# Kernel optimization log

Measured on AMD Instinct MI355X. Metric: run time of the kernel, lower is better.

The kernel has to match this reference:

```python
import jax, jax.numpy as jnp
import numpy as np

N_NODES = 100000
N_EDGES = 1600000
MSG = 128
EPS = 1e-12  # F.normalize default eps


def setup_inputs() -> dict:
    key = jax.random.key(0)
    ks = jax.random.split(key, 12)
    s = 1.0 / np.sqrt(MSG)
    inp = {
        "x": jax.random.normal(ks[0], (N_NODES, 3), dtype=jnp.float32),
        "m_ij": jax.random.normal(ks[1], (N_EDGES, MSG), dtype=jnp.float32),
        "edges": jax.random.randint(ks[2], (2, N_EDGES), 0, N_NODES, dtype=jnp.int64),
        # weigths MLP: Linear(MSG,MSG) -> SiLU -> Linear(MSG,1)
        "Ww1": jax.random.uniform(ks[3], (MSG, MSG), jnp.float32, -s, s),
        "bw1": jax.random.uniform(ks[4], (MSG,), jnp.float32, -s, s),
        "Ww2": jax.random.uniform(ks[5], (MSG, 1), jnp.float32, -s, s),
        "bw2": jax.random.uniform(ks[6], (1,), jnp.float32, -s, s),
        # attention MLP: Linear(MSG,MSG) -> SiLU -> Linear(MSG,1)
        "Wa1": jax.random.uniform(ks[7], (MSG, MSG), jnp.float32, -s, s),
        "ba1": jax.random.uniform(ks[8], (MSG,), jnp.float32, -s, s),
        "Wa2": jax.random.uniform(ks[9], (MSG, 1), jnp.float32, -s, s),
        "ba2": jax.random.uniform(ks[10], (1,), jnp.float32, -s, s),
    }
    return inp


def reference(x, m_ij, edges, Ww1, bw1, Ww2, bw2, Wa1, ba1, Wa2, ba2):
    n_nodes = x.shape[0]
    src = edges[0]  # receiver index (scatter target)
    dst = edges[1]  # neighbor index

    # w_ij = MLP(m_ij) -> [E, 1]
    w_ij = jax.nn.silu(m_ij @ Ww1 + bw1) @ Ww2 + bw2

    # attention: a_ij = exp(MLP(m_ij)); normalized per receiver node (softmax-like)
    a_ij = jnp.exp(jax.nn.silu(m_ij @ Wa1 + ba1) @ Wa2 + ba2)  # [E, 1]
    a_i = jax.ops.segment_sum(a_ij, src, num_segments=n_nodes)  # [N, 1]
    w_ij = w_ij * (a_ij / a_i[src])

    # normalized position differences, weighted
    d = x[dst] - x[src]  # [E, 3]
    norm = jnp.maximum(jnp.linalg.norm(d, axis=1, keepdims=True), EPS)
    x_ij = (d / norm) * w_ij

    x_diff = jax.ops.segment_sum(x_ij, src, num_segments=n_nodes)  # [N, 3]
    return x + x_diff
```

## Files before the change

### kernel.cpp

```cpp
#include <hip/hip_runtime.h>
#include <cmath>

#define MSG 128
#define TILE_M 128

typedef __attribute__((ext_vector_type(8))) __bf16 bf16x8;
typedef __attribute__((ext_vector_type(4))) float f32x4;

__device__ __forceinline__ unsigned short f2bf(float f) {
  union { float f; unsigned u; } v; v.f = f;
  unsigned r = v.u + 0x7FFFu + ((v.u >> 16) & 1u);
  return (unsigned short)(r >> 16);
}

__global__ void prep_weights_kernel(const float* __restrict__ Ww1,
                                    const float* __restrict__ Wa1,
                                    unsigned short* __restrict__ WtW,
                                    unsigned short* __restrict__ WtA) {
  int idx = blockIdx.x * blockDim.x + threadIdx.x;
  if (idx < MSG * MSG) {
    int k = idx >> 7;
    int n = idx & 127;
    WtW[n * MSG + k] = f2bf(Ww1[idx]);
    WtA[n * MSG + k] = f2bf(Wa1[idx]);
  }
}

__global__ __launch_bounds__(256, 5)
void edge_mlp_fused_kernel(const float* __restrict__ m_ij,
                           const unsigned short* __restrict__ WtW,
                           const unsigned short* __restrict__ WtA,
                           const float* __restrict__ bw1, const float* __restrict__ Ww2,
                           const float* __restrict__ bw2,
                           const float* __restrict__ ba1, const float* __restrict__ Wa2,
                           const float* __restrict__ ba2,
                           const int* __restrict__ src,
                           const int* __restrict__ dst,
                           const float* __restrict__ x,
                           float* __restrict__ num4, int E) {
  const int tid = threadIdx.x;
  const int wv = tid >> 6;
  const int lane = tid & 63;
  const int quad = lane >> 4;
  const int l16 = lane & 15;
  const int ebase = blockIdx.x * TILE_M + wv * 32;

  const int eown = ebase + lane;
  const bool owner = (lane < 32) && (eown < E);
  int s = 0, d = 0;
  if (owner) { s = src[eown]; d = dst[eown]; }

  bf16x8 mfrag[2][4];
  #pragma unroll
  for (int et = 0; et < 2; ++et) {
    int e = ebase + et * 16 + l16;
    if (e >= E) e = E - 1;
    const float* row = m_ij + (size_t)e * MSG + quad * 8;
    #pragma unroll
    for (int kt = 0; kt < 4; ++kt) {
      const float4 v0 = *(const float4*)(row + kt * 32);
      const float4 v1 = *(const float4*)(row + kt * 32 + 4);
      bf16x8 f;
      f[0] = (__bf16)v0.x; f[1] = (__bf16)v0.y;
      f[2] = (__bf16)v0.z; f[3] = (__bf16)v0.w;
      f[4] = (__bf16)v1.x; f[5] = (__bf16)v1.y;
      f[6] = (__bf16)v1.z; f[7] = (__bf16)v1.w;
      mfrag[et][kt] = f;
    }
  }

  float sx = 0.f, sy = 0.f, sz = 0.f, gx = 0.f, gy = 0.f, gz = 0.f;
  if (owner) {
    sx = x[3 * s];     sy = x[3 * s + 1]; sz = x[3 * s + 2];
    gx = x[3 * d];     gy = x[3 * d + 1]; gz = x[3 * d + 2];
  }

  float pW0 = 0.f, pW1 = 0.f, pA0 = 0.f, pA1 = 0.f;
  #pragma unroll
  for (int nt = 0; nt < 8; ++nt) {
    const size_t ro = (size_t)(nt * 16 + l16) * MSG + quad * 8;
    f32x4 aw0 = {0.f, 0.f, 0.f, 0.f}, aw1 = {0.f, 0.f, 0.f, 0.f};
    f32x4 aa0 = {0.f, 0.f, 0.f, 0.f}, aa1 = {0.f, 0.f, 0.f, 0.f};
    #pragma unroll
    for (int kt = 0; kt < 4; ++kt) {
      const bf16x8 Aw = *(const bf16x8*)(WtW + ro + kt * 32);
      const bf16x8 Aa = *(const bf16x8*)(WtA + ro + kt * 32);
      aw0 = __builtin_amdgcn_mfma_f32_16x16x32_bf16(Aw, mfrag[0][kt], aw0, 0, 0, 0);
      aw1 = __builtin_amdgcn_mfma_f32_16x16x32_bf16(Aw, mfrag[1][kt], aw1, 0, 0, 0);
      aa0 = __builtin_amdgcn_mfma_f32_16x16x32_bf16(Aa, mfrag[0][kt], aa0, 0, 0, 0);
      aa1 = __builtin_amdgcn_mfma_f32_16x16x32_bf16(Aa, mfrag[1][kt], aa1, 0, 0, 0);
    }
    const f32x4 bwq = *(const f32x4*)(bw1 + nt * 16 + quad * 4);
    const f32x4 wwq = *(const f32x4*)(Ww2 + nt * 16 + quad * 4);
    const f32x4 baq = *(const f32x4*)(ba1 + nt * 16 + quad * 4);
    const f32x4 waq = *(const f32x4*)(Wa2 + nt * 16 + quad * 4);
    #pragma unroll
    for (int r = 0; r < 4; ++r) {
      const float hw0 = aw0[r] + bwq[r];
      const float hw1 = aw1[r] + bwq[r];
      const float ha0 = aa0[r] + baq[r];
      const float ha1 = aa1[r] + baq[r];
      pW0 += (hw0 * wwq[r]) * __builtin_amdgcn_rcpf(1.f + __expf(-hw0));
      pW1 += (hw1 * wwq[r]) * __builtin_amdgcn_rcpf(1.f + __expf(-hw1));
      pA0 += (ha0 * waq[r]) * __builtin_amdgcn_rcpf(1.f + __expf(-ha0));
      pA1 += (ha1 * waq[r]) * __builtin_amdgcn_rcpf(1.f + __expf(-ha1));
    }
  }
  pW0 += __shfl_xor(pW0, 16, 64); pW0 += __shfl_xor(pW0, 32, 64);
  pW1 += __shfl_xor(pW1, 16, 64); pW1 += __shfl_xor(pW1, 32, 64);
  pA0 += __shfl_xor(pA0, 16, 64); pA0 += __shfl_xor(pA0, 32, 64);
  pA1 += __shfl_xor(pA1, 16, 64); pA1 += __shfl_xor(pA1, 32, 64);

  if (owner) {
    const float vW = ((lane < 16) ? pW0 : pW1) + bw2[0];
    const float vA = ((lane < 16) ? pA0 : pA1) + ba2[0];
    const float a = __expf(vA);
    const float t = vW * a;
    const float dx = gx - sx, dy = gy - sy, dz = gz - sz;
    const float nrm = sqrtf(dx * dx + dy * dy + dz * dz);
    const float inv = t * __builtin_amdgcn_rcpf(fmaxf(nrm, 1e-12f));
    float* base = num4 + (size_t)4 * s;
    atomicAdd(base + 0, dx * inv);
    atomicAdd(base + 1, dy * inv);
    atomicAdd(base + 2, dz * inv);
    atomicAdd(base + 3, a);
  }
}

__global__ void finalize_kernel(const float* __restrict__ x,
                                const f32x4* __restrict__ num4,
                                float* __restrict__ out, int N) {
  int n = blockIdx.x * blockDim.x + threadIdx.x;
  if (n >= N) return;
  const f32x4 v = num4[n];
  const float inv = (v[3] != 0.f) ? __builtin_amdgcn_rcpf(v[3]) : 0.f;
  out[3 * n + 0] = x[3 * n + 0] + v[0] * inv;
  out[3 * n + 1] = x[3 * n + 1] + v[1] * inv;
  out[3 * n + 2] = x[3 * n + 2] + v[2] * inv;
}

extern "C" void kernel_launch(void* const* d_in, const int* in_sizes, int n_in,
                              void* d_out, int out_size, void* d_ws, size_t ws_size,
                              hipStream_t stream) {
  const float* x    = (const float*)d_in[0];
  const float* m_ij = (const float*)d_in[1];
  const int*   edges = (const int*)d_in[2];
  const float* Ww1 = (const float*)d_in[3];
  const float* bw1 = (const float*)d_in[4];
  const float* Ww2 = (const float*)d_in[5];
  const float* bw2 = (const float*)d_in[6];
  const float* Wa1 = (const float*)d_in[7];
  const float* ba1 = (const float*)d_in[8];
  const float* Wa2 = (const float*)d_in[9];
  const float* ba2 = (const float*)d_in[10];

  const int N = in_sizes[0] / 3;
  const int E = in_sizes[1] / MSG;
  const int* src = edges;
  const int* dst = edges + E;

  char* p = (char*)d_ws;
  unsigned short* WtW = (unsigned short*)p; p += (size_t)MSG * MSG * 2;
  unsigned short* WtA = (unsigned short*)p; p += (size_t)MSG * MSG * 2;
  float* num4 = (float*)p; p += (size_t)N * 4 * 4;

  float* out = (float*)d_out;

  hipMemsetAsync(num4, 0, (size_t)N * 4 * 4, stream);
  prep_weights_kernel<<<(MSG * MSG + 255) / 256, 256, 0, stream>>>(Ww1, Wa1, WtW, WtA);
  edge_mlp_fused_kernel<<<(E + TILE_M - 1) / TILE_M, 256, 0, stream>>>(
      m_ij, WtW, WtA, bw1, Ww2, bw2, ba1, Wa2, ba2, src, dst, x, num4, E);
  finalize_kernel<<<(N + 255) / 256, 256, 0, stream>>>(x, (const f32x4*)num4, out, N);
}
```

Before: 1.428 ms.

## Persistent double-buffered edge MLP kernel with register-resident weights and async LDS loads

Replaces the one-tile-per-block edge MLP kernel with a persistent grid of at most 512 blocks. Each block streams 64-edge tiles of m_ij into a double-buffered, XOR-swizzled LDS buffer using global_load_lds, so the next tile's load overlaps the current tile's MFMA work. Each wave now keeps its slice of the two weight matrices and bias vectors in registers instead of re-reading them from global memory for every tile. The per-wave partial dot products are combined across waves through LDS before the atomic scatter. The cost is lower occupancy, extra barriers per tile, and hand-written vmcnt waits that depend on the order in which memory operations are issued.

```diff
diff --git a/kernel.cpp b/kernel.cpp
--- a/kernel.cpp
+++ b/kernel.cpp
@@ -2,7 +2,9 @@
 #include <cmath>
 
 #define MSG 128
-#define TILE_M 128
+#define TILE 64
+#define TPB 256
+#define NB_MAX 512
 
 typedef __attribute__((ext_vector_type(8))) __bf16 bf16x8;
 typedef __attribute__((ext_vector_type(4))) float f32x4;
@@ -26,104 +28,160 @@
   }
 }
 
-__global__ __launch_bounds__(256, 5)
-void edge_mlp_fused_kernel(const float* __restrict__ m_ij,
-                           const unsigned short* __restrict__ WtW,
-                           const unsigned short* __restrict__ WtA,
-                           const float* __restrict__ bw1, const float* __restrict__ Ww2,
-                           const float* __restrict__ bw2,
-                           const float* __restrict__ ba1, const float* __restrict__ Wa2,
-                           const float* __restrict__ ba2,
-                           const int* __restrict__ src,
-                           const int* __restrict__ dst,
-                           const float* __restrict__ x,
-                           float* __restrict__ num4, int E) {
+__device__ __forceinline__ void gload_lds16(const float* g, float* l) {
+  __builtin_amdgcn_global_load_lds(
+      (const __attribute__((address_space(1))) void*)g,
+      (__attribute__((address_space(3))) void*)l, 16, 0, 0);
+}
+
+__global__ __launch_bounds__(TPB, 2)
+void edge_mlp_pipe_kernel(const float* __restrict__ m_ij,
+                          const unsigned short* __restrict__ WtW,
+                          const unsigned short* __restrict__ WtA,
+                          const float* __restrict__ bw1, const float* __restrict__ Ww2,
+                          const float* __restrict__ bw2,
+                          const float* __restrict__ ba1, const float* __restrict__ Wa2,
+                          const float* __restrict__ ba2,
+                          const int* __restrict__ src,
+                          const int* __restrict__ dst,
+                          const float* __restrict__ x,
+                          float* __restrict__ num4, int E, int ntiles) {
+  __shared__ __align__(16) float buf[2][TILE * MSG];
+  __shared__ float plds[2][4][TILE];
+
   const int tid = threadIdx.x;
-  const int wv = tid >> 6;
+  const int w = tid >> 6;
   const int lane = tid & 63;
   const int quad = lane >> 4;
   const int l16 = lane & 15;
-  const int ebase = blockIdx.x * TILE_M + wv * 32;
-
-  const int eown = ebase + lane;
-  const bool owner = (lane < 32) && (eown < E);
-  int s = 0, d = 0;
-  if (owner) { s = src[eown]; d = dst[eown]; }
-
-  bf16x8 mfrag[2][4];
+
+  bf16x8 wf[2][2][4];
+  f32x4 c1[2][2], c2[2][2];
   #pragma unroll
-  for (int et = 0; et < 2; ++et) {
-    int e = ebase + et * 16 + l16;
-    if (e >= E) e = E - 1;
-    const float* row = m_ij + (size_t)e * MSG + quad * 8;
+  for (int nt = 0; nt < 2; ++nt) {
+    const int unit16 = w * 32 + nt * 16;
+    const size_t ro = (size_t)(unit16 + l16) * MSG + quad * 8;
     #pragma unroll
     for (int kt = 0; kt < 4; ++kt) {
-      const float4 v0 = *(const float4*)(row + kt * 32);
-      const float4 v1 = *(const float4*)(row + kt * 32 + 4);
-      bf16x8 f;
-      f[0] = (__bf16)v0.x; f[1] = (__bf16)v0.y;
-      f[2] = (__bf16)v0.z; f[3] = (__bf16)v0.w;
-      f[4] = (__bf16)v1.x; f[5] = (__bf16)v1.y;
-      f[6] = (__bf16)v1.z; f[7] = (__bf16)v1.w;
-      mfrag[et][kt] = f;
-    }
+      wf[nt][0][kt] = *(const bf16x8*)(WtW + ro + kt * 32);
+      wf[nt][1][kt] = *(const bf16x8*)(WtA + ro + kt * 32);
+    }
+    const int co = unit16 + quad * 4;
+    c1[nt][0] = *(const f32x4*)(bw1 + co);
+    c2[nt][0] = *(const f32x4*)(Ww2 + co);
+    c1[nt][1] = *(const f32x4*)(ba1 + co);
+    c2[nt][1] = *(const f32x4*)(Wa2 + co);
   }
-
-  float sx = 0.f, sy = 0.f, sz = 0.f, gx = 0.f, gy = 0.f, gz = 0.f;
-  if (owner) {
-    sx = x[3 * s];     sy = x[3 * s + 1]; sz = x[3 * s + 2];
-    gx = x[3 * d];     gy = x[3 * d + 1]; gz = x[3 * d + 2];
-  }
-
-  float pW0 = 0.f, pW1 = 0.f, pA0 = 0.f, pA1 = 0.f;
-  #pragma unroll
-  for (int nt = 0; nt < 8; ++nt) {
-    const size_t ro = (size_t)(nt * 16 + l16) * MSG + quad * 8;
-    f32x4 aw0 = {0.f, 0.f, 0.f, 0.f}, aw1 = {0.f, 0.f, 0.f, 0.f};
-    f32x4 aa0 = {0.f, 0.f, 0.f, 0.f}, aa1 = {0.f, 0.f, 0.f, 0.f};
+  const float bw2s = bw2[0], ba2s = ba2[0];
+
+  auto stage = [&](int tile, int bsel) {
     #pragma unroll
-    for (int kt = 0; kt < 4; ++kt) {
-      const bf16x8 Aw = *(const bf16x8*)(WtW + ro + kt * 32);
-      const bf16x8 Aa = *(const bf16x8*)(WtA + ro + kt * 32);
-      aw0 = __builtin_amdgcn_mfma_f32_16x16x32_bf16(Aw, mfrag[0][kt], aw0, 0, 0, 0);
-      aw1 = __builtin_amdgcn_mfma_f32_16x16x32_bf16(Aw, mfrag[1][kt], aw1, 0, 0, 0);
-      aa0 = __builtin_amdgcn_mfma_f32_16x16x32_bf16(Aa, mfrag[0][kt], aa0, 0, 0, 0);
-      aa1 = __builtin_amdgcn_mfma_f32_16x16x32_bf16(Aa, mfrag[1][kt], aa1, 0, 0, 0);
-    }
-    const f32x4 bwq = *(const f32x4*)(bw1 + nt * 16 + quad * 4);
-    const f32x4 wwq = *(const f32x4*)(Ww2 + nt * 16 + quad * 4);
-    const f32x4 baq = *(const f32x4*)(ba1 + nt * 16 + quad * 4);
-    const f32x4 waq = *(const f32x4*)(Wa2 + nt * 16 + quad * 4);
+    for (int i = 0; i < 8; ++i) {
+      const int chunk = i * TPB + tid;
+      const int db = chunk * 16;
+      const int row = db >> 9;
+      const int col = db & 511;
+      const int scol = col ^ ((row & 7) << 4);
+      int grow = tile * TILE + row;
+      if (grow >= E) grow = E - 1;
+      const float* g = m_ij + (size_t)grow * MSG + (scol >> 2);
+      gload_lds16(g, &buf[bsel][0] + (db >> 2));
+    }
+  };
+
+  int tt = blockIdx.x;
+  if (tt < ntiles) stage(tt, 0);
+  asm volatile("s_waitcnt vmcnt(0)" ::: "memory");
+  __builtin_amdgcn_s_barrier();
+  int cur = 0;
+
+  for (; tt < ntiles; tt += gridDim.x) {
+    const int nxt = tt + (int)gridDim.x;
+    if (nxt < ntiles) stage(nxt, cur ^ 1);
+
+    const int eL = w * 16 + l16;
+    const int ge = tt * TILE + eL;
+    const bool fown = (quad == 0) && (ge < E);
+    int sN = 0, dN = 0;
+    float sx = 0.f, sy = 0.f, sz = 0.f, gx = 0.f, gy = 0.f, gz = 0.f;
+    if (fown) { sN = src[ge]; dN = dst[ge]; }
+    if (fown) {
+      sx = x[3 * sN]; sy = x[3 * sN + 1]; sz = x[3 * sN + 2];
+      gx = x[3 * dN]; gy = x[3 * dN + 1]; gz = x[3 * dN + 2];
+    }
+
     #pragma unroll
-    for (int r = 0; r < 4; ++r) {
-      const float hw0 = aw0[r] + bwq[r];
-      const float hw1 = aw1[r] + bwq[r];
-      const float ha0 = aa0[r] + baq[r];
-      const float ha1 = aa1[r] + baq[r];
-      pW0 += (hw0 * wwq[r]) * __builtin_amdgcn_rcpf(1.f + __expf(-hw0));
-      pW1 += (hw1 * wwq[r]) * __builtin_amdgcn_rcpf(1.f + __expf(-hw1));
-      pA0 += (ha0 * waq[r]) * __builtin_amdgcn_rcpf(1.f + __expf(-ha0));
-      pA1 += (ha1 * waq[r]) * __builtin_amdgcn_rcpf(1.f + __expf(-ha1));
-    }
-  }
-  pW0 += __shfl_xor(pW0, 16, 64); pW0 += __shfl_xor(pW0, 32, 64);
-  pW1 += __shfl_xor(pW1, 16, 64); pW1 += __shfl_xor(pW1, 32, 64);
-  pA0 += __shfl_xor(pA0, 16, 64); pA0 += __shfl_xor(pA0, 32, 64);
-  pA1 += __shfl_xor(pA1, 16, 64); pA1 += __shfl_xor(pA1, 32, 64);
-
-  if (owner) {
-    const float vW = ((lane < 16) ? pW0 : pW1) + bw2[0];
-    const float vA = ((lane < 16) ? pA0 : pA1) + ba2[0];
-    const float a = __expf(vA);
-    const float t = vW * a;
-    const float dx = gx - sx, dy = gy - sy, dz = gz - sz;
-    const float nrm = sqrtf(dx * dx + dy * dy + dz * dz);
-    const float inv = t * __builtin_amdgcn_rcpf(fmaxf(nrm, 1e-12f));
-    float* base = num4 + (size_t)4 * s;
-    atomicAdd(base + 0, dx * inv);
-    atomicAdd(base + 1, dy * inv);
-    atomicAdd(base + 2, dz * inv);
-    atomicAdd(base + 3, a);
+    for (int et = 0; et < 4; ++et) {
+      const int row = et * 16 + l16;
+      const int rbase = row * MSG;
+      const int xorf = (row & 7) << 2;
+      bf16x8 bf[4];
+      #pragma unroll
+      for (int kt = 0; kt < 4; ++kt) {
+        const int c0 = quad * 8 + kt * 32;
+        const f32x4 v0 = *(const f32x4*)(&buf[cur][rbase + (c0 ^ xorf)]);
+        const f32x4 v1 = *(const f32x4*)(&buf[cur][rbase + ((c0 + 4) ^ xorf)]);
+        bf16x8 f;
+        f[0] = (__bf16)v0.x; f[1] = (__bf16)v0.y;
+        f[2] = (__bf16)v0.z; f[3] = (__bf16)v0.w;
+        f[4] = (__bf16)v1.x; f[5] = (__bf16)v1.y;
+        f[6] = (__bf16)v1.z; f[7] = (__bf16)v1.w;
+        bf[kt] = f;
+      }
+      f32x4 acc[2][2];
+      #pragma unroll
+      for (int nt = 0; nt < 2; ++nt) {
+        acc[nt][0] = {0.f, 0.f, 0.f, 0.f};
+        acc[nt][1] = {0.f, 0.f, 0.f, 0.f};
+      }
+      #pragma unroll
+      for (int kt = 0; kt < 4; ++kt) {
+        #pragma unroll
+        for (int nt = 0; nt < 2; ++nt) {
+          acc[nt][0] = __builtin_amdgcn_mfma_f32_16x16x32_bf16(wf[nt][0][kt], bf[kt], acc[nt][0], 0, 0, 0);
+          acc[nt][1] = __builtin_amdgcn_mfma_f32_16x16x32_bf16(wf[nt][1][kt], bf[kt], acc[nt][1], 0, 0, 0);
+        }
+      }
+      float pW = 0.f, pA = 0.f;
+      #pragma unroll
+      for (int nt = 0; nt < 2; ++nt) {
+        #pragma unroll
+        for (int r = 0; r < 4; ++r) {
+          const float hw = acc[nt][0][r] + c1[nt][0][r];
+          const float ha = acc[nt][1][r] + c1[nt][1][r];
+          pW += (hw * c2[nt][0][r]) * __builtin_amdgcn_rcpf(1.f + __expf(-hw));
+          pA += (ha * c2[nt][1][r]) * __builtin_amdgcn_rcpf(1.f + __expf(-ha));
+        }
+      }
+      pW += __shfl_xor(pW, 16, 64); pW += __shfl_xor(pW, 32, 64);
+      pA += __shfl_xor(pA, 16, 64); pA += __shfl_xor(pA, 32, 64);
+      if (quad == 0) {
+        plds[0][w][et * 16 + l16] = pW;
+        plds[1][w][et * 16 + l16] = pA;
+      }
+    }
+
+    asm volatile("s_waitcnt lgkmcnt(0)" ::: "memory");
+    __builtin_amdgcn_s_barrier();
+
+    if (fown) {
+      const float sW = plds[0][0][eL] + plds[0][1][eL] + plds[0][2][eL] + plds[0][3][eL];
+      const float sA = plds[1][0][eL] + plds[1][1][eL] + plds[1][2][eL] + plds[1][3][eL];
+      const float a = __expf(sA + ba2s);
+      const float t = (sW + bw2s) * a;
+      const float dx = gx - sx, dy = gy - sy, dz = gz - sz;
+      const float nrm = sqrtf(dx * dx + dy * dy + dz * dz);
+      const float inv = t * __builtin_amdgcn_rcpf(fmaxf(nrm, 1e-12f));
+      float* basep = num4 + (size_t)4 * sN;
+      atomicAdd(basep + 0, dx * inv);
+      atomicAdd(basep + 1, dy * inv);
+      atomicAdd(basep + 2, dz * inv);
+      atomicAdd(basep + 3, a);
+    }
+
+    asm volatile("s_waitcnt vmcnt(4) lgkmcnt(0)" ::: "memory");
+    __builtin_amdgcn_s_barrier();
+    cur ^= 1;
   }
 }
 
@@ -166,9 +224,12 @@
 
   float* out = (float*)d_out;
 
+  const int ntiles = (E + TILE - 1) / TILE;
+  const int nb = ntiles < NB_MAX ? ntiles : NB_MAX;
+
   hipMemsetAsync(num4, 0, (size_t)N * 4 * 4, stream);
   prep_weights_kernel<<<(MSG * MSG + 255) / 256, 256, 0, stream>>>(Ww1, Wa1, WtW, WtA);
-  edge_mlp_fused_kernel<<<(E + TILE_M - 1) / TILE_M, 256, 0, stream>>>(
-      m_ij, WtW, WtA, bw1, Ww2, bw2, ba1, Wa2, ba2, src, dst, x, num4, E);
+  edge_mlp_pipe_kernel<<<nb, TPB, 0, stream>>>(
+      m_ij, WtW, WtA, bw1, Ww2, bw2, ba1, Wa2, ba2, src, dst, x, num4, E, ntiles);
   finalize_kernel<<<(N + 255) / 256, 256, 0, stream>>>(x, (const f32x4*)num4, out, N);
 }
```

Result: faster. 1.238 ms (-13.3%).
